# Kernel optimization log

Measured on AMD Instinct MI355X. Metric: run time of the kernel, lower is better.

The kernel has to match this reference:

```python
import jax, jax.numpy as jnp
import numpy as np

EMB, HID, NH = 512, 256, 8
DH = HID // NH
LN_EPS = 1e-5


def _mk(key, shape, scale=0.02):
    return jax.random.normal(key, shape, dtype=jnp.float32) * scale


def setup_inputs() -> dict:
    key = jax.random.key(0)
    ks = jax.random.split(key, 24)
    B, S = 8, 256
    return {
        "memory_embeddings": jax.random.normal(ks[0], (B, S, EMB), dtype=jnp.float32),
        # memory_encoder: Linear(512,256) -> LayerNorm -> ReLU -> Linear(256,256)
        "enc_w1": _mk(ks[1], (HID, EMB)), "enc_b1": jnp.zeros((HID,), jnp.float32),
        "ln_g": jnp.ones((HID,), jnp.float32), "ln_b": jnp.zeros((HID,), jnp.float32),
        "enc_w2": _mk(ks[2], (HID, HID)), "enc_b2": jnp.zeros((HID,), jnp.float32),
        # MultiheadAttention packed qkv + out proj
        "in_proj_w": _mk(ks[3], (3 * HID, HID)), "in_proj_b": jnp.zeros((3 * HID,), jnp.float32),
        "out_w": _mk(ks[4], (HID, HID)), "out_b": jnp.zeros((HID,), jnp.float32),
        # consistency head: Linear(256,128) -> ReLU -> Linear(128,1) -> Sigmoid
        "cons_w1": _mk(ks[5], (HID // 2, HID)), "cons_b1": jnp.zeros((HID // 2,), jnp.float32),
        "cons_w2": _mk(ks[6], (1, HID // 2)), "cons_b2": jnp.zeros((1,), jnp.float32),
        # hallucination detector
        "hall_w1": _mk(ks[7], (HID // 2, HID)), "hall_b1": jnp.zeros((HID // 2,), jnp.float32),
        "hall_w2": _mk(ks[8], (1, HID // 2)), "hall_b2": jnp.zeros((1,), jnp.float32),
        # contradiction analyzer: Linear(512,256) -> ReLU -> Linear(256,1) -> Sigmoid
        "con_w1": _mk(ks[9], (HID, 2 * HID)), "con_b1": jnp.zeros((HID,), jnp.float32),
        "con_w2": _mk(ks[10], (1, HID)), "con_b2": jnp.zeros((1,), jnp.float32),
    }


def _forward(memory_embeddings, enc_w1, enc_b1, ln_g, ln_b, enc_w2, enc_b2,
             in_proj_w, in_proj_b, out_w, out_b,
             cons_w1, cons_b1, cons_w2, cons_b2,
             hall_w1, hall_b1, hall_w2, hall_b2,
             con_w1, con_b1, con_w2, con_b2):
    B, S, _ = memory_embeddings.shape
    # --- memory encoder (dropout in eval mode = identity) ---
    h = memory_embeddings @ enc_w1.T + enc_b1                      # [B,S,HID]
    mu = h.mean(-1, keepdims=True)
    var = ((h - mu) ** 2).mean(-1, keepdims=True)
    h = (h - mu) * jax.lax.rsqrt(var + LN_EPS) * ln_g + ln_b
    mf = jax.nn.relu(h) @ enc_w2.T + enc_b2                        # [B,S,HID]
    # --- multihead self-attention (batch_first, averaged attn weights) ---
    qkv = mf @ in_proj_w.T + in_proj_b                              # [B,S,3H]
    q, k, v = jnp.split(qkv, 3, axis=-1)
    def heads(t):  # [B,S,H] -> [B,NH,S,DH]
        return t.reshape(B, S, NH, DH).transpose(0, 2, 1, 3)
    q, k, v = heads(q), heads(k), heads(v)
    scores = jnp.einsum('bhsd,bhtd->bhst', q, k) / jnp.sqrt(jnp.float32(DH))
    attn = jax.nn.softmax(scores, axis=-1)                          # [B,NH,S,S]
    ctx = jnp.einsum('bhst,bhtd->bhsd', attn, v)
    ctx = ctx.transpose(0, 2, 1, 3).reshape(B, S, HID)
    attended = ctx @ out_w.T + out_b                                # [B,S,HID]
    attn_weights = attn.mean(axis=1)                                # [B,S,S]
    # --- pooled heads ---
    pooled = attended.mean(axis=1)                                  # [B,HID]
    cons = jax.nn.sigmoid(jax.nn.relu(pooled @ cons_w1.T + cons_b1) @ cons_w2.T + cons_b2)[:, 0]
    hall = jax.nn.sigmoid(jax.nn.relu(pooled @ hall_w1.T + hall_b1) @ hall_w2.T + hall_b2)[:, 0]
    # --- contradiction matrix over all i<j pairs (vectorized gather/MLP/scatter) ---
    iu, ju = np.triu_indices(S, k=1)                                # static indices
    Wa, Wb = con_w1[:, :HID], con_w1[:, HID:]                       # split concat-linear
    a = mf @ Wa.T                                                   # [B,S,HID]
    b = mf @ Wb.T
    hid = jax.nn.relu(a[:, iu] + b[:, ju] + con_b1)                 # [B,P,HID]
    sc = jax.nn.sigmoid(hid @ con_w2.T + con_b2)[..., 0]            # [B,P]
    M = jnp.zeros((B, S, S), dtype=mf.dtype)
    M = M.at[:, iu, ju].set(sc)
    M = M.at[:, ju, iu].set(sc)
    return cons, hall, M, attn_weights


def reference(memory_embeddings, enc_w1, enc_b1, ln_g, ln_b, enc_w2, enc_b2,
              in_proj_w, in_proj_b, out_w, out_b,
              cons_w1, cons_b1, cons_w2, cons_b2,
              hall_w1, hall_b1, hall_w2, hall_b2,
              con_w1, con_b1, con_w2, con_b2):
    return _forward(memory_embeddings, enc_w1, enc_b1, ln_g, ln_b, enc_w2, enc_b2,
                    in_proj_w, in_proj_b, out_w, out_b,
                    cons_w1, cons_b1, cons_w2, cons_b2,
                    hall_w1, hall_b1, hall_w2, hall_b2,
                    con_w1, con_b1, con_w2, con_b2)
```

## Files before the change

kernel.cpp:

```cpp
#include <hip/hip_runtime.h>
#include <math.h>

typedef __attribute__((ext_vector_type(8))) short bf16x8;
typedef __attribute__((ext_vector_type(4))) float f32x4;

__device__ __forceinline__ short f2b(float f) {
  union { float f; unsigned u; } v; v.f = f;
  unsigned u = v.u + 0x7fffu + ((v.u >> 16) & 1u);
  return (short)(u >> 16);
}

__device__ __forceinline__ bf16x8 cvt8(float4 a, float4 b) {
  bf16x8 r;
  r[0] = f2b(a.x); r[1] = f2b(a.y); r[2] = f2b(a.z); r[3] = f2b(a.w);
  r[4] = f2b(b.x); r[5] = f2b(b.y); r[6] = f2b(b.z); r[7] = f2b(b.w);
  return r;
}

__global__ __launch_bounds__(512) void k_enc(
    const float* __restrict__ me,
    const float* __restrict__ w1f, const float* __restrict__ b1,
    const float* __restrict__ g, const float* __restrict__ lb,
    const float* __restrict__ w2f, const float* __restrict__ b2,
    const float* __restrict__ in_proj_w, const float* __restrict__ con_w1,
    unsigned short* __restrict__ mfb, unsigned short* __restrict__ wbf,
    float* __restrict__ poolctx, float* __restrict__ out_aw) {
  __shared__ float hh[16 * 260];
  __shared__ unsigned short rA[16 * 264];
  __shared__ unsigned short mfs[16 * 256];
  int tid = threadIdx.x;
  if (blockIdx.x >= 128) {
    int cidx = (blockIdx.x - 128) * 512 + tid;
    if (cidx < 65536) {
      float4 z = {0.f, 0.f, 0.f, 0.f};
      float4* aw4 = (float4*)out_aw;
      aw4[cidx * 2] = z;
      aw4[cidx * 2 + 1] = z;
    }
    int base = cidx * 4;
#pragma unroll
    for (int u = 0; u < 4; ++u) {
      int idx = base + u;
      float v;
      if (idx < 196608) v = in_proj_w[idx];
      else {
        int i = idx - 196608, n = i >> 8, k = i & 255;
        v = (n < 256) ? con_w1[n * 512 + k] : con_w1[(n - 256) * 512 + 256 + k];
      }
      wbf[idx] = (unsigned short)f2b(v);
    }
    return;
  }
  int lane = tid & 63, w = tid >> 6;
  int row0 = blockIdx.x * 16;
  int m = lane & 15, q = lane >> 4;
  if (blockIdx.x == 0) {
    float4 z = {0.f, 0.f, 0.f, 0.f};
    ((float4*)poolctx)[tid] = z;
  }
  {
    f32x4 acc0 = (f32x4){0.f, 0.f, 0.f, 0.f};
    f32x4 acc1 = (f32x4){0.f, 0.f, 0.f, 0.f};
    const float* ap = me + (size_t)(row0 + m) * 512 + q * 8;
    const float* bp0 = w1f + (size_t)(w * 32 + m) * 512 + q * 8;
    const float* bp1 = w1f + (size_t)(w * 32 + 16 + m) * 512 + q * 8;
    float4 pa[4][2], pb[4][2][2];
#pragma unroll
    for (int d = 0; d < 4; ++d) {
      pa[d][0] = *(const float4*)(ap + d * 32);
      pa[d][1] = *(const float4*)(ap + d * 32 + 4);
      pb[d][0][0] = *(const float4*)(bp0 + d * 32);
      pb[d][0][1] = *(const float4*)(bp0 + d * 32 + 4);
      pb[d][1][0] = *(const float4*)(bp1 + d * 32);
      pb[d][1][1] = *(const float4*)(bp1 + d * 32 + 4);
    }
#pragma unroll
    for (int it = 0; it < 16; ++it) {
      int slot = it & 3;
      float4 a0 = pa[slot][0], a1 = pa[slot][1];
      float4 b00 = pb[slot][0][0], b01 = pb[slot][0][1];
      float4 b10 = pb[slot][1][0], b11 = pb[slot][1][1];
      if (it + 4 < 16) {
        pa[slot][0] = *(const float4*)(ap + (it + 4) * 32);
        pa[slot][1] = *(const float4*)(ap + (it + 4) * 32 + 4);
        pb[slot][0][0] = *(const float4*)(bp0 + (it + 4) * 32);
        pb[slot][0][1] = *(const float4*)(bp0 + (it + 4) * 32 + 4);
        pb[slot][1][0] = *(const float4*)(bp1 + (it + 4) * 32);
        pb[slot][1][1] = *(const float4*)(bp1 + (it + 4) * 32 + 4);
      }
      bf16x8 af = cvt8(a0, a1);
      acc0 = __builtin_amdgcn_mfma_f32_16x16x32_bf16(af, cvt8(b00, b01), acc0, 0, 0, 0);
      acc1 = __builtin_amdgcn_mfma_f32_16x16x32_bf16(af, cvt8(b10, b11), acc1, 0, 0, 0);
    }
#pragma unroll
    for (int nt = 0; nt < 2; ++nt) {
      int col = w * 32 + nt * 16 + m;
      float bias = b1[col];
      f32x4 a = nt ? acc1 : acc0;
#pragma unroll
      for (int reg = 0; reg < 4; ++reg)
        hh[(q * 4 + reg) * 260 + col] = a[reg] + bias;
    }
  }
  __syncthreads();
  {
    float4 g4 = *(const float4*)(g + lane * 4);
    float4 lb4 = *(const float4*)(lb + lane * 4);
#pragma unroll
    for (int rr = 0; rr < 2; ++rr) {
      int r = w * 2 + rr;
      float4 v = *(const float4*)&hh[r * 260 + lane * 4];
      float s1 = v.x + v.y + v.z + v.w;
      float s2 = v.x * v.x + v.y * v.y + v.z * v.z + v.w * v.w;
#pragma unroll
      for (int o = 32; o > 0; o >>= 1) {
        s1 += __shfl_xor(s1, o, 64);
        s2 += __shfl_xor(s2, o, 64);
      }
      float mu = s1 * (1.f / 256.f);
      float var = s2 * (1.f / 256.f) - mu * mu;
      float rs = rsqrtf(var + 1e-5f);
      unsigned short y0 = (unsigned short)f2b(fmaxf((v.x - mu) * rs * g4.x + lb4.x, 0.f));
      unsigned short y1 = (unsigned short)f2b(fmaxf((v.y - mu) * rs * g4.y + lb4.y, 0.f));
      unsigned short y2 = (unsigned short)f2b(fmaxf((v.z - mu) * rs * g4.z + lb4.z, 0.f));
      unsigned short y3 = (unsigned short)f2b(fmaxf((v.w - mu) * rs * g4.w + lb4.w, 0.f));
      uint2 pk;
      pk.x = (unsigned)y0 | ((unsigned)y1 << 16);
      pk.y = (unsigned)y2 | ((unsigned)y3 << 16);
      *(uint2*)&rA[r * 264 + lane * 4] = pk;
    }
  }
  __syncthreads();
  {
    f32x4 acc0 = (f32x4){0.f, 0.f, 0.f, 0.f};
    f32x4 acc1 = (f32x4){0.f, 0.f, 0.f, 0.f};
    const float* cp0 = w2f + (size_t)(w * 32 + m) * 256 + q * 8;
    const float* cp1 = w2f + (size_t)(w * 32 + 16 + m) * 256 + q * 8;
    float4 pb[4][2][2];
#pragma unroll
    for (int d = 0; d < 4; ++d) {
      pb[d][0][0] = *(const float4*)(cp0 + d * 32);
      pb[d][0][1] = *(const float4*)(cp0 + d * 32 + 4);
      pb[d][1][0] = *(const float4*)(cp1 + d * 32);
      pb[d][1][1] = *(const float4*)(cp1 + d * 32 + 4);
    }
#pragma unroll
    for (int it = 0; it < 8; ++it) {
      int slot = it & 3;
      float4 b00 = pb[slot][0][0], b01 = pb[slot][0][1];
      float4 b10 = pb[slot][1][0], b11 = pb[slot][1][1];
      if (it + 4 < 8) {
        pb[slot][0][0] = *(const float4*)(cp0 + (it + 4) * 32);
        pb[slot][0][1] = *(const float4*)(cp0 + (it + 4) * 32 + 4);
        pb[slot][1][0] = *(const float4*)(cp1 + (it + 4) * 32);
        pb[slot][1][1] = *(const float4*)(cp1 + (it + 4) * 32 + 4);
      }
      bf16x8 af = *(const bf16x8*)&rA[m * 264 + it * 32 + q * 8];
      acc0 = __builtin_amdgcn_mfma_f32_16x16x32_bf16(af, cvt8(b00, b01), acc0, 0, 0, 0);
      acc1 = __builtin_amdgcn_mfma_f32_16x16x32_bf16(af, cvt8(b10, b11), acc1, 0, 0, 0);
    }
#pragma unroll
    for (int nt = 0; nt < 2; ++nt) {
      int col = w * 32 + nt * 16 + m;
      float bias = b2[col];
      f32x4 a = nt ? acc1 : acc0;
#pragma unroll
      for (int reg = 0; reg < 4; ++reg)
        mfs[(q * 4 + reg) * 256 + col] = (unsigned short)f2b(a[reg] + bias);
    }
  }
  __syncthreads();
  {
    const uint4* src = (const uint4*)mfs;
    uint4* dst = (uint4*)(mfb + (size_t)row0 * 256);
    dst[tid] = src[tid];
  }
}

__global__ __launch_bounds__(256) void k_proj5(
    const unsigned short* __restrict__ mfb,
    const unsigned short* __restrict__ wbf,
    const float* __restrict__ bq, const float* __restrict__ cb1,
    float* __restrict__ qh, float* __restrict__ kh, float* __restrict__ vh,
    float* __restrict__ amat, float* __restrict__ bmat) {
  int tid = threadIdx.x, lane = tid & 63, w = tid >> 6;
  int row0 = blockIdx.x * 16;
  int part = blockIdx.y;
  int m = lane & 15, q = lane >> 4;
  const unsigned short* W = wbf + (size_t)part * 65536;
  bf16x8 a[8];
#pragma unroll
  for (int ks = 0; ks < 8; ++ks)
    a[ks] = *(const bf16x8*)(mfb + (size_t)(row0 + m) * 256 + ks * 32 + q * 8);
  f32x4 acc[4];
#pragma unroll
  for (int i = 0; i < 4; ++i) acc[i] = (f32x4){0.f, 0.f, 0.f, 0.f};
  bf16x8 pb[4][4];
#pragma unroll
  for (int d = 0; d < 4; ++d)
#pragma unroll
    for (int nt = 0; nt < 4; ++nt)
      pb[d][nt] = *(const bf16x8*)(W + (size_t)(w * 64 + nt * 16 + m) * 256 + d * 32 + q * 8);
#pragma unroll
  for (int it = 0; it < 8; ++it) {
    int slot = it & 3;
    bf16x8 bl0 = pb[slot][0], bl1 = pb[slot][1];
    bf16x8 bl2 = pb[slot][2], bl3 = pb[slot][3];
    if (it + 4 < 8) {
#pragma unroll
      for (int nt = 0; nt < 4; ++nt)
        pb[slot][nt] = *(const bf16x8*)(W + (size_t)(w * 64 + nt * 16 + m) * 256 + (it + 4) * 32 + q * 8);
    }
    acc[0] = __builtin_amdgcn_mfma_f32_16x16x32_bf16(a[it], bl0, acc[0], 0, 0, 0);
    acc[1] = __builtin_amdgcn_mfma_f32_16x16x32_bf16(a[it], bl1, acc[1], 0, 0, 0);
    acc[2] = __builtin_amdgcn_mfma_f32_16x16x32_bf16(a[it], bl2, acc[2], 0, 0, 0);
    acc[3] = __builtin_amdgcn_mfma_f32_16x16x32_bf16(a[it], bl3, acc[3], 0, 0, 0);
  }
#pragma unroll
  for (int nt = 0; nt < 4; ++nt) {
    int col = w * 64 + nt * 16 + m;
    if (part < 3) {
      float bias = bq[part * 256 + col];
      float* dst = (part == 0) ? qh : (part == 1) ? kh : vh;
      int h = col >> 5, d = col & 31;
#pragma unroll
      for (int reg = 0; reg < 4; ++reg) {
        int row = row0 + q * 4 + reg;
        int b = row >> 8, s = row & 255;
        dst[(((size_t)(b * 8 + h)) * 256 + s) * 32 + d] = acc[nt][reg] + bias;
      }
    } else {
      float bias = (part == 3) ? cb1[col] : 0.f;
      float* dst = (part == 3) ? amat : bmat;
#pragma unroll
      for (int reg = 0; reg < 4; ++reg) {
        int row = row0 + q * 4 + reg;
        dst[(size_t)row * 256 + col] = acc[nt][reg] + bias;
      }
    }
  }
}

__global__ __launch_bounds__(256) void k_attn_pairs(
    const float* __restrict__ qh, const float* __restrict__ kh,
    const float* __restrict__ vh, float* __restrict__ out_aw,
    float* __restrict__ poolctx,
    const float* __restrict__ amat, const float* __restrict__ bmat,
    const float* __restrict__ conw2, const float* __restrict__ conb2,
    float* __restrict__ M) {
  __shared__ __align__(16) char smem_raw[57856];
  int bx = blockIdx.x, tid = threadIdx.x;
  if (bx < 512) {
    unsigned short* qs = (unsigned short*)smem_raw;
    unsigned short* kb = qs + 1280;
    unsigned short* vt = qs + 11520;
    unsigned short* ps = qs + 19968;
    float* redm = (float*)(smem_raw + 56832);
    float* reds = redm + 64;
    int sg = bx & 7, bh = bx >> 3, h = bh & 7, b = bh >> 3;
    int lane = tid & 63, w = tid >> 6;
    int m = lane & 15, q = lane >> 4;
    {
      const float* qbase = qh + (((size_t)bh) * 256 + sg * 32) * 32;
      float4 v = ((const float4*)qbase)[tid];
      int r = tid >> 3, c4 = tid & 7;
      unsigned short* dst = &qs[r * 40 + c4 * 4];
      dst[0] = (unsigned short)f2b(v.x); dst[1] = (unsigned short)f2b(v.y);
      dst[2] = (unsigned short)f2b(v.z); dst[3] = (unsigned short)f2b(v.w);
    }
    {
      const float4* kbase = (const float4*)(kh + ((size_t)bh) * 256 * 32);
#pragma unroll
      for (int i = 0; i < 8; ++i) {
        int f = i * 256 + tid;
        float4 v = kbase[f];
        int r = f >> 3, c4 = f & 7;
        unsigned short* dst = &kb[r * 40 + c4 * 4];
        dst[0] = (unsigned short)f2b(v.x); dst[1] = (unsigned short)f2b(v.y);
        dst[2] = (unsigned short)f2b(v.z); dst[3] = (unsigned short)f2b(v.w);
      }
    }
    {
      const float4* vr = (const float4*)(vh + (((size_t)bh) * 256 + tid) * 32);
#pragma unroll
      for (int d4 = 0; d4 < 8; ++d4) {
        float4 vv = vr[d4];
        vt[(d4 * 4 + 0) * 264 + tid] = (unsigned short)f2b(vv.x);
        vt[(d4 * 4 + 1) * 264 + tid] = (unsigned short)f2b(vv.y);
        vt[(d4 * 4 + 2) * 264 + tid] = (unsigned short)f2b(vv.z);
        vt[(d4 * 4 + 3) * 264 + tid] = (unsigned short)f2b(vv.w);
      }
    }
    __syncthreads();
    int mt = w & 1, ng = w >> 1;
    int lrow = mt * 16 + q * 4;
    f32x4 acc[8];
    {
      bf16x8 af = *(const bf16x8*)&qs[(mt * 16 + m) * 40 + q * 8];
#pragma unroll
      for (int nt = 0; nt < 8; ++nt) {
        bf16x8 bf = *(const bf16x8*)&kb[(ng * 128 + nt * 16 + m) * 40 + q * 8];
        acc[nt] = __builtin_amdgcn_mfma_f32_16x16x32_bf16(
            af, bf, (f32x4){0.f, 0.f, 0.f, 0.f}, 0, 0, 0);
      }
    }
    const float scale = 0.17677669529663689f;
#pragma unroll
    for (int nt = 0; nt < 8; ++nt)
#pragma unroll
      for (int reg = 0; reg < 4; ++reg) acc[nt][reg] *= scale;
    float pm[4];
#pragma unroll
    for (int reg = 0; reg < 4; ++reg) {
      float mx = acc[0][reg];
#pragma unroll
      for (int nt = 1; nt < 8; ++nt) mx = fmaxf(mx, acc[nt][reg]);
#pragma unroll
      for (int o = 1; o < 16; o <<= 1) mx = fmaxf(mx, __shfl_xor(mx, o, 64));
      pm[reg] = mx;
    }
    if (m == 0) {
#pragma unroll
      for (int reg = 0; reg < 4; ++reg) redm[ng * 32 + lrow + reg] = pm[reg];
    }
    __syncthreads();
    float inv[4], psum[4];
#pragma unroll
    for (int reg = 0; reg < 4; ++reg) {
      float Mv = fmaxf(redm[lrow + reg], redm[32 + lrow + reg]);
      float s = 0.f;
#pragma unroll
      for (int nt = 0; nt < 8; ++nt) {
        float e = __expf(acc[nt][reg] - Mv);
        acc[nt][reg] = e;
        s += e;
      }
#pragma unroll
      for (int o = 1; o < 16; o <<= 1) s += __shfl_xor(s, o, 64);
      psum[reg] = s;
    }
    if (m == 0) {
#pragma unroll
      for (int reg = 0; reg < 4; ++reg) reds[ng * 32 + lrow + reg] = psum[reg];
    }
    __syncthreads();
#pragma unroll
    for (int reg = 0; reg < 4; ++reg)
      inv[reg] = 1.f / (reds[lrow + reg] + reds[32 + lrow + reg]);
    float* awb = out_aw + ((size_t)b << 16);
#pragma unroll
    for (int nt = 0; nt < 8; ++nt) {
      int t = ng * 128 + nt * 16 + m;
#pragma unroll
      for (int reg = 0; reg < 4; ++reg) {
        float p = acc[nt][reg] * inv[reg];
        ps[(lrow + reg) * 264 + t] = (unsigned short)f2b(p);
        atomicAdd(awb + (sg * 32 + lrow + reg) * 256 + t, p * 0.125f);
      }
    }
    __syncthreads();
    {
      int dt = w >> 1;
      f32x4 a = (f32x4){0.f, 0.f, 0.f, 0.f};
#pragma unroll
      for (int ks = 0; ks < 256; ks += 32) {
        bf16x8 af = *(const bf16x8*)&ps[(mt * 16 + m) * 264 + ks + q * 8];
        bf16x8 bf = *(const bf16x8*)&vt[(dt * 16 + m) * 264 + ks + q * 8];
        a = __builtin_amdgcn_mfma_f32_16x16x32_bf16(af, bf, a, 0, 0, 0);
      }
      float colsum = a[0] + a[1] + a[2] + a[3];
      colsum += __shfl_xor(colsum, 16, 64);
      colsum += __shfl_xor(colsum, 32, 64);
      if (lane < 16)
        atomicAdd(&poolctx[b * 256 + h * 32 + dt * 16 + m], colsum);
    }
  } else {
    float* As = (float*)smem_raw;
    float* Bs = As + 16 * 132;
    float* w2s = As + 16 * 132 + 32 * 132;
    int u = bx - 512;
    int b = u / 72, r2 = u % 72;
    int tix = r2 >> 1, half = r2 & 1;
    int it = 0, rem = tix;
    while (rem >= 8 - it) { rem -= 8 - it; ++it; }
    int jt = it + rem;
    int ti = tid >> 4, tj = tid & 15;
    w2s[tid] = conw2[tid];
    float acc00 = 0, acc01 = 0;
    const float* Ab = amat + ((size_t)(b * 256 + it * 32 + half * 16)) * 256;
    const float* Bb = bmat + ((size_t)(b * 256 + jt * 32)) * 256;
    for (int ch = 0; ch < 2; ++ch) {
      __syncthreads();
#pragma unroll
      for (int k = 0; k < 2; ++k) {
        int f = tid + k * 256;
        int r = f >> 5, c4 = f & 31;
        *(float4*)&As[r * 132 + c4 * 4] =
            *(const float4*)(Ab + (size_t)r * 256 + ch * 128 + c4 * 4);
      }
#pragma unroll
      for (int k = 0; k < 4; ++k) {
        int f = tid + k * 256;
        int r = f >> 5, c4 = f & 31;
        *(float4*)&Bs[r * 132 + c4 * 4] =
            *(const float4*)(Bb + (size_t)r * 256 + ch * 128 + c4 * 4);
      }
      __syncthreads();
      const float* a0 = As + ti * 132;
      const float* b0 = Bs + (2 * tj) * 132;
      const float* b1 = b0 + 132;
      const float* w2c = w2s + ch * 128;
      for (int d = 0; d < 128; d += 4) {
        float4 wv = *(const float4*)&w2c[d];
        float4 av = *(const float4*)&a0[d];
        float4 bv0 = *(const float4*)&b0[d];
        float4 bv1 = *(const float4*)&b1[d];
        acc00 += fmaxf(av.x + bv0.x, 0.f) * wv.x + fmaxf(av.y + bv0.y, 0.f) * wv.y
               + fmaxf(av.z + bv0.z, 0.f) * wv.z + fmaxf(av.w + bv0.w, 0.f) * wv.w;
        acc01 += fmaxf(av.x + bv1.x, 0.f) * wv.x + fmaxf(av.y + bv1.y, 0.f) * wv.y
               + fmaxf(av.z + bv1.z, 0.f) * wv.z + fmaxf(av.w + bv1.w, 0.f) * wv.w;
      }
    }
    float c2 = conb2[0];
    float s00 = 1.f / (1.f + expf(-(acc00 + c2)));
    float s01 = 1.f / (1.f + expf(-(acc01 + c2)));
    float* Mb = M + ((size_t)b << 16);
    int i0 = it * 32 + half * 16 + ti;
    int j0 = jt * 32 + 2 * tj, j1 = j0 + 1;
    if (it != jt) {
      Mb[i0 * 256 + j0] = s00; Mb[j0 * 256 + i0] = s00;
      Mb[i0 * 256 + j1] = s01; Mb[j1 * 256 + i0] = s01;
    } else {
      if (j0 > i0) { Mb[i0 * 256 + j0] = s00; Mb[j0 * 256 + i0] = s00; }
      else if (j0 == i0) Mb[i0 * 256 + j0] = 0.f;
      if (j1 > i0) { Mb[i0 * 256 + j1] = s01; Mb[j1 * 256 + i0] = s01; }
      else if (j1 == i0) Mb[i0 * 256 + j1] = 0.f;
    }
  }
}

__global__ __launch_bounds__(256) void k_heads(
    const float* __restrict__ poolctx,
    const float* __restrict__ outw, const float* __restrict__ outb,
    const float* __restrict__ cw1, const float* __restrict__ cb1h,
    const float* __restrict__ cw2, const float* __restrict__ cb2,
    const float* __restrict__ hw1, const float* __restrict__ hb1,
    const float* __restrict__ hw2, const float* __restrict__ hb2,
    float* __restrict__ out) {
  __shared__ float pc[256];
  __shared__ float psh[256];
  __shared__ float red[4];
  int b = blockIdx.x, j = threadIdx.x;
  pc[j] = poolctx[b * 256 + j] * (1.f / 256.f);
  __syncthreads();
  float s = outb[j];
  const float4* wr = (const float4*)(outw + (size_t)j * 256);
  for (int k4 = 0; k4 < 64; ++k4) {
    float4 wv = wr[k4];
    const float* p = pc + k4 * 4;
    s += p[0] * wv.x + p[1] * wv.y + p[2] * wv.z + p[3] * wv.w;
  }
  psh[j] = s;
  __syncthreads();
  int jj = j & 127;
  bool isH = j >= 128;
  const float* w1 = isH ? hw1 : cw1;
  const float* bb1 = isH ? hb1 : cb1h;
  const float* w2 = isH ? hw2 : cw2;
  float a = bb1[jj];
  const float4* w1r = (const float4*)(w1 + (size_t)jj * 256);
  for (int k4 = 0; k4 < 64; ++k4) {
    float4 wv = w1r[k4];
    const float* p = psh + k4 * 4;
    a += p[0] * wv.x + p[1] * wv.y + p[2] * wv.z + p[3] * wv.w;
  }
  float v = fmaxf(a, 0.f) * w2[jj];
#pragma unroll
  for (int o = 32; o > 0; o >>= 1) v += __shfl_xor(v, o, 64);
  if ((j & 63) == 0) red[j >> 6] = v;
  __syncthreads();
  if (j == 0) {
    float c = red[0] + red[1] + cb2[0];
    float h = red[2] + red[3] + hb2[0];
    out[b] = 1.f / (1.f + expf(-c));
    out[8 + b] = 1.f / (1.f + expf(-h));
  }
}

extern "C" void kernel_launch(void* const* d_in, const int* in_sizes, int n_in,
                              void* d_out, int out_size, void* d_ws, size_t ws_size,
                              hipStream_t stream) {
  const float* me        = (const float*)d_in[0];
  const float* enc_w1    = (const float*)d_in[1];
  const float* enc_b1    = (const float*)d_in[2];
  const float* ln_g      = (const float*)d_in[3];
  const float* ln_b      = (const float*)d_in[4];
  const float* enc_w2    = (const float*)d_in[5];
  const float* enc_b2    = (const float*)d_in[6];
  const float* in_proj_w = (const float*)d_in[7];
  const float* in_proj_b = (const float*)d_in[8];
  const float* out_w     = (const float*)d_in[9];
  const float* out_b     = (const float*)d_in[10];
  const float* cons_w1   = (const float*)d_in[11];
  const float* cons_b1   = (const float*)d_in[12];
  const float* cons_w2   = (const float*)d_in[13];
  const float* cons_b2   = (const float*)d_in[14];
  const float* hall_w1   = (const float*)d_in[15];
  const float* hall_b1   = (const float*)d_in[16];
  const float* hall_w2   = (const float*)d_in[17];
  const float* hall_b2   = (const float*)d_in[18];
  const float* con_w1    = (const float*)d_in[19];
  const float* con_b1    = (const float*)d_in[20];
  const float* con_w2    = (const float*)d_in[21];
  const float* con_b2    = (const float*)d_in[22];

  float* ws = (float*)d_ws;
  float* qh   = ws;
  float* kh   = ws + 524288;
  float* vh   = ws + 1048576;
  float* amat = ws + 1572864;
  float* bmat = ws + 2097152;
  unsigned short* mfb = (unsigned short*)(ws + 2621440);
  unsigned short* wbf = (unsigned short*)(ws + 2883584);
  float* poolctx = ws + 3047424;

  float* out    = (float*)d_out;
  float* out_M  = out + 16;
  float* out_aw = out + 16 + 524288;

  k_enc<<<288, 512, 0, stream>>>(me, enc_w1, enc_b1, ln_g, ln_b,
                                 enc_w2, enc_b2, in_proj_w, con_w1,
                                 mfb, wbf, poolctx, out_aw);
  k_proj5<<<dim3(128, 5), 256, 0, stream>>>(mfb, wbf, in_proj_b, con_b1,
                                            qh, kh, vh, amat, bmat);
  k_attn_pairs<<<1088, 256, 0, stream>>>(qh, kh, vh, out_aw, poolctx,
                                         amat, bmat, con_w2, con_b2, out_M);
  k_heads<<<8, 256, 0, stream>>>(poolctx, out_w, out_b,
                                 cons_w1, cons_b1, cons_w2, cons_b2,
                                 hall_w1, hall_b1, hall_w2, hall_b2, out);
}
```

Measured before the change: 201.3 us.

## Replace atomic head-averaged attention writes with bf16 staging and a reduction pass

The attention kernel no longer performs a float atomicAdd per probability into the averaged attention-weights output. Each head now writes its bf16 probability tile to a workspace buffer with vectorized stores. A new tail kernel sums the eight heads per batch and writes the averaged result, and it also runs the heads MLP in extra blocks. This removes about half a million contended global atomics and the zero-fill of the output, at the cost of an extra 8 MB round trip through memory and some loss of precision from summing bf16 values.

```diff
diff --git a/kernel.cpp b/kernel.cpp
--- a/kernel.cpp
+++ b/kernel.cpp
@@ -24,20 +24,13 @@
     const float* __restrict__ w2f, const float* __restrict__ b2,
     const float* __restrict__ in_proj_w, const float* __restrict__ con_w1,
     unsigned short* __restrict__ mfb, unsigned short* __restrict__ wbf,
-    float* __restrict__ poolctx, float* __restrict__ out_aw) {
+    float* __restrict__ poolctx) {
   __shared__ float hh[16 * 260];
   __shared__ unsigned short rA[16 * 264];
   __shared__ unsigned short mfs[16 * 256];
   int tid = threadIdx.x;
   if (blockIdx.x >= 128) {
-    int cidx = (blockIdx.x - 128) * 512 + tid;
-    if (cidx < 65536) {
-      float4 z = {0.f, 0.f, 0.f, 0.f};
-      float4* aw4 = (float4*)out_aw;
-      aw4[cidx * 2] = z;
-      aw4[cidx * 2 + 1] = z;
-    }
-    int base = cidx * 4;
+    int base = ((blockIdx.x - 128) * 512 + tid) * 4;
 #pragma unroll
     for (int u = 0; u < 4; ++u) {
       int idx = base + u;
@@ -243,7 +236,7 @@
 
 __global__ __launch_bounds__(256) void k_attn_pairs(
     const float* __restrict__ qh, const float* __restrict__ kh,
-    const float* __restrict__ vh, float* __restrict__ out_aw,
+    const float* __restrict__ vh, unsigned short* __restrict__ attnb,
     float* __restrict__ poolctx,
     const float* __restrict__ amat, const float* __restrict__ bmat,
     const float* __restrict__ conw2, const float* __restrict__ conb2,
@@ -347,18 +340,20 @@
 #pragma unroll
     for (int reg = 0; reg < 4; ++reg)
       inv[reg] = 1.f / (reds[lrow + reg] + reds[32 + lrow + reg]);
-    float* awb = out_aw + ((size_t)b << 16);
 #pragma unroll
     for (int nt = 0; nt < 8; ++nt) {
       int t = ng * 128 + nt * 16 + m;
 #pragma unroll
-      for (int reg = 0; reg < 4; ++reg) {
-        float p = acc[nt][reg] * inv[reg];
-        ps[(lrow + reg) * 264 + t] = (unsigned short)f2b(p);
-        atomicAdd(awb + (sg * 32 + lrow + reg) * 256 + t, p * 0.125f);
-      }
-    }
-    __syncthreads();
+      for (int reg = 0; reg < 4; ++reg)
+        ps[(lrow + reg) * 264 + t] = (unsigned short)f2b(acc[nt][reg] * inv[reg]);
+    }
+    __syncthreads();
+    {
+      int r = tid >> 3, seg = tid & 7;
+      const uint4* src = (const uint4*)&ps[r * 264 + seg * 32];
+      uint4* dst = (uint4*)(attnb + ((size_t)(bh * 256 + sg * 32 + r)) * 256 + seg * 32);
+      dst[0] = src[0]; dst[1] = src[1]; dst[2] = src[2]; dst[3] = src[3];
+    }
     {
       int dt = w >> 1;
       f32x4 a = (f32x4){0.f, 0.f, 0.f, 0.f};
@@ -439,7 +434,8 @@
   }
 }
 
-__global__ __launch_bounds__(256) void k_heads(
+__global__ __launch_bounds__(256) void k_tail2(
+    const unsigned short* __restrict__ attnb, float* __restrict__ out_aw,
     const float* __restrict__ poolctx,
     const float* __restrict__ outw, const float* __restrict__ outb,
     const float* __restrict__ cw1, const float* __restrict__ cb1h,
@@ -450,40 +446,61 @@
   __shared__ float pc[256];
   __shared__ float psh[256];
   __shared__ float red[4];
-  int b = blockIdx.x, j = threadIdx.x;
-  pc[j] = poolctx[b * 256 + j] * (1.f / 256.f);
-  __syncthreads();
-  float s = outb[j];
-  const float4* wr = (const float4*)(outw + (size_t)j * 256);
-  for (int k4 = 0; k4 < 64; ++k4) {
-    float4 wv = wr[k4];
-    const float* p = pc + k4 * 4;
-    s += p[0] * wv.x + p[1] * wv.y + p[2] * wv.z + p[3] * wv.w;
-  }
-  psh[j] = s;
-  __syncthreads();
-  int jj = j & 127;
-  bool isH = j >= 128;
-  const float* w1 = isH ? hw1 : cw1;
-  const float* bb1 = isH ? hb1 : cb1h;
-  const float* w2 = isH ? hw2 : cw2;
-  float a = bb1[jj];
-  const float4* w1r = (const float4*)(w1 + (size_t)jj * 256);
-  for (int k4 = 0; k4 < 64; ++k4) {
-    float4 wv = w1r[k4];
-    const float* p = psh + k4 * 4;
-    a += p[0] * wv.x + p[1] * wv.y + p[2] * wv.z + p[3] * wv.w;
-  }
-  float v = fmaxf(a, 0.f) * w2[jj];
-#pragma unroll
-  for (int o = 32; o > 0; o >>= 1) v += __shfl_xor(v, o, 64);
-  if ((j & 63) == 0) red[j >> 6] = v;
-  __syncthreads();
-  if (j == 0) {
-    float c = red[0] + red[1] + cb2[0];
-    float h = red[2] + red[3] + hb2[0];
-    out[b] = 1.f / (1.f + expf(-c));
-    out[8 + b] = 1.f / (1.f + expf(-h));
+  int bx = blockIdx.x, tid = threadIdx.x;
+  if (bx < 256) {
+    int gid = bx * 256 + tid;
+    int b = gid >> 13, e8 = gid & 8191;
+    size_t e = (size_t)e8 * 8;
+    float s0 = 0, s1 = 0, s2 = 0, s3 = 0, s4 = 0, s5 = 0, s6 = 0, s7 = 0;
+#pragma unroll
+    for (int h = 0; h < 8; ++h) {
+      uint4 v = *(const uint4*)(attnb + (((size_t)(b * 8 + h)) << 16) + e);
+      s0 += __uint_as_float(v.x << 16); s1 += __uint_as_float(v.x & 0xffff0000u);
+      s2 += __uint_as_float(v.y << 16); s3 += __uint_as_float(v.y & 0xffff0000u);
+      s4 += __uint_as_float(v.z << 16); s5 += __uint_as_float(v.z & 0xffff0000u);
+      s6 += __uint_as_float(v.w << 16); s7 += __uint_as_float(v.w & 0xffff0000u);
+    }
+    float* dst = out_aw + ((size_t)b << 16) + e;
+    float4 r0 = {s0 * 0.125f, s1 * 0.125f, s2 * 0.125f, s3 * 0.125f};
+    float4 r1 = {s4 * 0.125f, s5 * 0.125f, s6 * 0.125f, s7 * 0.125f};
+    *(float4*)dst = r0;
+    *(float4*)(dst + 4) = r1;
+  } else {
+    int b = bx - 256, j = tid;
+    pc[j] = poolctx[b * 256 + j] * (1.f / 256.f);
+    __syncthreads();
+    float s = outb[j];
+    const float4* wr = (const float4*)(outw + (size_t)j * 256);
+    for (int k4 = 0; k4 < 64; ++k4) {
+      float4 wv = wr[k4];
+      const float* p = pc + k4 * 4;
+      s += p[0] * wv.x + p[1] * wv.y + p[2] * wv.z + p[3] * wv.w;
+    }
+    psh[j] = s;
+    __syncthreads();
+    int jj = j & 127;
+    bool isH = j >= 128;
+    const float* w1 = isH ? hw1 : cw1;
+    const float* bb1 = isH ? hb1 : cb1h;
+    const float* w2 = isH ? hw2 : cw2;
+    float a = bb1[jj];
+    const float4* w1r = (const float4*)(w1 + (size_t)jj * 256);
+    for (int k4 = 0; k4 < 64; ++k4) {
+      float4 wv = w1r[k4];
+      const float* p = psh + k4 * 4;
+      a += p[0] * wv.x + p[1] * wv.y + p[2] * wv.z + p[3] * wv.w;
+    }
+    float v = fmaxf(a, 0.f) * w2[jj];
+#pragma unroll
+    for (int o = 32; o > 0; o >>= 1) v += __shfl_xor(v, o, 64);
+    if ((j & 63) == 0) red[j >> 6] = v;
+    __syncthreads();
+    if (j == 0) {
+      float c = red[0] + red[1] + cb2[0];
+      float h = red[2] + red[3] + hb2[0];
+      out[b] = 1.f / (1.f + expf(-c));
+      out[8 + b] = 1.f / (1.f + expf(-h));
+    }
   }
 }
 
@@ -518,11 +535,12 @@
   float* qh   = ws;
   float* kh   = ws + 524288;
   float* vh   = ws + 1048576;
-  float* amat = ws + 1572864;
-  float* bmat = ws + 2097152;
-  unsigned short* mfb = (unsigned short*)(ws + 2621440);
-  unsigned short* wbf = (unsigned short*)(ws + 2883584);
-  float* poolctx = ws + 3047424;
+  unsigned short* attnb = (unsigned short*)(ws + 1572864);
+  float* amat = ws + 3670016;
+  float* bmat = ws + 4194304;
+  unsigned short* mfb = (unsigned short*)(ws + 4718592);
+  unsigned short* wbf = (unsigned short*)(ws + 4980736);
+  float* poolctx = ws + 5144576;
 
   float* out    = (float*)d_out;
   float* out_M  = out + 16;
@@ -530,12 +548,13 @@
 
   k_enc<<<288, 512, 0, stream>>>(me, enc_w1, enc_b1, ln_g, ln_b,
                                  enc_w2, enc_b2, in_proj_w, con_w1,
-                                 mfb, wbf, poolctx, out_aw);
+                                 mfb, wbf, poolctx);
   k_proj5<<<dim3(128, 5), 256, 0, stream>>>(mfb, wbf, in_proj_b, con_b1,
                                             qh, kh, vh, amat, bmat);
-  k_attn_pairs<<<1088, 256, 0, stream>>>(qh, kh, vh, out_aw, poolctx,
+  k_attn_pairs<<<1088, 256, 0, stream>>>(qh, kh, vh, attnb, poolctx,
                                          amat, bmat, con_w2, con_b2, out_M);
-  k_heads<<<8, 256, 0, stream>>>(poolctx, out_w, out_b,
-                                 cons_w1, cons_b1, cons_w2, cons_b2,
-                                 hall_w1, hall_b1, hall_w2, hall_b2, out);
-}
+  k_tail2<<<264, 256, 0, stream>>>(attnb, out_aw, poolctx,
+                                   out_w, out_b,
+                                   cons_w1, cons_b1, cons_w2, cons_b2,
+                                   hall_w1, hall_b1, hall_w2, hall_b2, out);
+}
```

New measurement: 189.9 us. 1.06x faster.
